# Optimization experiments

Measured on AMD Instinct MI355X. Metric: run time of the kernel, lower is better.

Reference implementation:

```python
import jax, jax.numpy as jnp
import numpy as np

N_QUBITS = 4
N_LAYERS = 2
BATCH = 1048576


def setup_inputs() -> dict:
    key = jax.random.key(0)
    k1, k2 = jax.random.split(key)
    noise = jax.random.normal(k1, (BATCH, N_QUBITS), dtype=jnp.float32)
    weights = jax.random.normal(k2, (N_LAYERS, N_QUBITS), dtype=jnp.float32)
    return {"noise": noise, "weights": weights}


def _apply_1q(state, U, wire):
    # state: (B, 2,2,2,2) complex; U: (2,2) or (B,2,2)
    s = jnp.moveaxis(state, wire + 1, -1)
    if U.ndim == 3:
        s = jnp.einsum('bij,b...j->b...i', U, s)
    else:
        s = jnp.einsum('ij,...j->...i', U, s)
    return jnp.moveaxis(s, -1, wire + 1)


def _apply_cnot(state, ctrl, tgt):
    ca, ta = ctrl + 1, tgt + 1
    s0 = jnp.take(state, 0, axis=ca)
    s1 = jnp.take(state, 1, axis=ca)
    ta_shift = ta if ta < ca else ta - 1  # target axis after removing ctrl axis
    s1 = jnp.flip(s1, axis=ta_shift)      # X on target when ctrl=1
    return jnp.stack([s0, s1], axis=ca)


def reference(noise, weights):
    B = noise.shape[0]
    # |0...0> initial state, shape (B, 2,2,2,2)
    state = jnp.zeros((B,) + (2,) * N_QUBITS, dtype=jnp.complex64)
    state = state.at[(slice(None),) + (0,) * N_QUBITS].set(1.0)

    # RX(noise[w]) on each wire (batched angles)
    for w in range(N_QUBITS):
        th = noise[:, w] * 0.5
        c, s = jnp.cos(th), jnp.sin(th)
        U = jnp.stack([jnp.stack([c + 0j, -1j * s], -1),
                       jnp.stack([-1j * s, c + 0j], -1)], -2).astype(jnp.complex64)
        state = _apply_1q(state, U, w)

    for layer in range(N_LAYERS):
        for w in range(N_QUBITS):
            state = _apply_cnot(state, w, (w + 1) % N_QUBITS)
        for w in range(N_QUBITS):
            th = weights[layer, w] * 0.5
            c, s = jnp.cos(th), jnp.sin(th)
            U = jnp.stack([jnp.stack([c, -s]), jnp.stack([s, c])]).astype(jnp.complex64)
            state = _apply_1q(state, U, w)

    probs = (state.real ** 2 + state.imag ** 2).astype(jnp.float32)
    cols = []
    for w in range(N_QUBITS):
        sum_axes = tuple(a for a in range(1, N_QUBITS + 1) if a != w + 1)
        marg = probs.sum(axis=sum_axes)  # (B, 2)
        # <Z> = p0 - p1, output = (<Z>+1)/2 = p0
        cols.append(marg[:, 0])
    return jnp.stack(cols, axis=-1)
```

## Files before the change

### kernel.cpp

```cpp
#include <hip/hip_runtime.h>
#include <math.h>


#define CNOT(cb, tb)                                                  \
    {                                                                 \
        _Pragma("unroll") for (int i = 0; i < 16; i++)                \
            if ((i & (cb)) && !(i & (tb))) {                          \
                int j = i | (tb);                                     \
                float t;                                              \
                t = re[i]; re[i] = re[j]; re[j] = t;                  \
                t = im[i]; im[i] = im[j]; im[j] = t;                  \
            }                                                         \
    }

#define RY(bit, cc, ss)                                               \
    {                                                                 \
        _Pragma("unroll") for (int i = 0; i < 16; i++)                \
            if (!(i & (bit))) {                                       \
                int j = i | (bit);                                    \
                float r0 = re[i], r1 = re[j];                         \
                float i0 = im[i], i1 = im[j];                         \
                re[i] = __builtin_fmaf((cc), r0, -((ss) * r1));       \
                re[j] = __builtin_fmaf((ss), r0, (cc) * r1);          \
                im[i] = __builtin_fmaf((cc), i0, -((ss) * i1));       \
                im[j] = __builtin_fmaf((ss), i0, (cc) * i1);          \
            }                                                         \
    }

__global__ __launch_bounds__(256) void qc_kernel(const float* __restrict__ noise,
                                                 const float* __restrict__ weights,
                                                 float* __restrict__ out, int B) {
    int b = blockIdx.x * blockDim.x + threadIdx.x;
    if (b >= B) return;

    float wc[8], wsn[8];
#pragma unroll
    for (int i = 0; i < 8; i++) {
        float th = weights[i] * 0.5f;
        __sincosf(th, &wsn[i], &wc[i]);
    }

    float4 nv = reinterpret_cast<const float4*>(noise)[b];
    float c0, s0, c1, s1, c2, s2, c3, s3;
    __sincosf(nv.x * 0.5f, &s0, &c0);
    __sincosf(nv.y * 0.5f, &s1, &c1);
    __sincosf(nv.z * 0.5f, &s2, &c2);
    __sincosf(nv.w * 0.5f, &s3, &c3);

    float m01[4], m23[4];
    m01[0] = c0 * c1; m01[1] = c0 * s1; m01[2] = s0 * c1; m01[3] = s0 * s1;
    m23[0] = c2 * c3; m23[1] = c2 * s3; m23[2] = s2 * c3; m23[3] = s2 * s3;

    float re[16], im[16];
#pragma unroll
    for (int i = 0; i < 16; i++) {
        float m = m01[i >> 2] * m23[i & 3];
        int pc = __popc(i) & 3;
        re[i] = (pc == 0) ? m : (pc == 2) ? -m : 0.0f;
        im[i] = (pc == 1) ? -m : (pc == 3) ? m : 0.0f;
    }

#pragma unroll
    for (int layer = 0; layer < 2; layer++) {
        CNOT(8, 4);
        CNOT(4, 2);
        CNOT(2, 1);
        CNOT(1, 8);
        RY(8, wc[layer * 4 + 0], wsn[layer * 4 + 0]);
        RY(4, wc[layer * 4 + 1], wsn[layer * 4 + 1]);
        RY(2, wc[layer * 4 + 2], wsn[layer * 4 + 2]);
        RY(1, wc[layer * 4 + 3], wsn[layer * 4 + 3]);
    }

    float p[16];
#pragma unroll
    for (int i = 0; i < 16; i++) p[i] = __builtin_fmaf(im[i], im[i], re[i] * re[i]);

    float g[4], h[4];
#pragma unroll
    for (int x = 0; x < 4; x++)
        g[x] = ((p[4 * x + 0] + p[4 * x + 1]) + (p[4 * x + 2] + p[4 * x + 3]));
#pragma unroll
    for (int y = 0; y < 4; y++)
        h[y] = ((p[y] + p[y + 4]) + (p[y + 8] + p[y + 12]));

    float o0 = g[0] + g[1];
    float o1 = g[0] + g[2];
    float o2 = h[0] + h[1];
    float o3 = h[0] + h[2];
    reinterpret_cast<float4*>(out)[b] = make_float4(o0, o1, o2, o3);
}

extern "C" void kernel_launch(void* const* d_in, const int* in_sizes, int n_in,
                              void* d_out, int out_size, void* d_ws, size_t ws_size,
                              hipStream_t stream) {
    const float* noise   = (const float*)d_in[0];
    const float* weights = (const float*)d_in[1];
    float* out = (float*)d_out;
    int B = in_sizes[0] / 4;

    qc_kernel<<<(B + 255) / 256, 256, 0, stream>>>(noise, weights, out, B);
}
```

Baseline: 79.88 us.

## Replace statevector simulation with closed-form expectation polynomials

Instead of simulating the 16-amplitude complex state through CNOT and RY gates, the kernel evaluates each qubit's <Z> as an analytic polynomial of the full-angle noise sines and cosines. Weight-dependent coefficients are combined into a few constants per output. This removes most per-thread arithmetic and register pressure, leaving the kernel dominated by memory traffic. The risk is correctness if the derived polynomial is wrong, and some numerical differences from reordering the arithmetic.

```diff
diff --git a/kernel.cpp b/kernel.cpp
--- a/kernel.cpp
+++ b/kernel.cpp
@@ -1,31 +1,6 @@
 #include <hip/hip_runtime.h>
 #include <math.h>
 
-
-#define CNOT(cb, tb)                                                  \
-    {                                                                 \
-        _Pragma("unroll") for (int i = 0; i < 16; i++)                \
-            if ((i & (cb)) && !(i & (tb))) {                          \
-                int j = i | (tb);                                     \
-                float t;                                              \
-                t = re[i]; re[i] = re[j]; re[j] = t;                  \
-                t = im[i]; im[i] = im[j]; im[j] = t;                  \
-            }                                                         \
-    }
-
-#define RY(bit, cc, ss)                                               \
-    {                                                                 \
-        _Pragma("unroll") for (int i = 0; i < 16; i++)                \
-            if (!(i & (bit))) {                                       \
-                int j = i | (bit);                                    \
-                float r0 = re[i], r1 = re[j];                         \
-                float i0 = im[i], i1 = im[j];                         \
-                re[i] = __builtin_fmaf((cc), r0, -((ss) * r1));       \
-                re[j] = __builtin_fmaf((ss), r0, (cc) * r1);          \
-                im[i] = __builtin_fmaf((cc), i0, -((ss) * i1));       \
-                im[j] = __builtin_fmaf((ss), i0, (cc) * i1);          \
-            }                                                         \
-    }
 
 __global__ __launch_bounds__(256) void qc_kernel(const float* __restrict__ noise,
                                                  const float* __restrict__ weights,
@@ -33,62 +8,74 @@
     int b = blockIdx.x * blockDim.x + threadIdx.x;
     if (b >= B) return;
 
-    float wc[8], wsn[8];
+    float C0[4], S0[4], C1[4], S1[4];
 #pragma unroll
-    for (int i = 0; i < 8; i++) {
-        float th = weights[i] * 0.5f;
-        __sincosf(th, &wsn[i], &wc[i]);
+    for (int v = 0; v < 4; v++) {
+        __sincosf(weights[v],     &S0[v], &C0[v]);
+        __sincosf(weights[4 + v], &S1[v], &C1[v]);
     }
 
+    float A0 = C1[0] * C0[3];
+    float K01 = A0 * C0[1] * C0[2], K02 = A0 * C0[1] * S0[2], K03 = -A0 * S0[1] * S0[2];
+    float K04 = S1[0] * C0[0] * S0[1], K05 = S1[0] * S0[0] * C0[1], K06 = -S1[0] * S0[0] * S0[1];
+
+    float K11 = C1[1] * C0[0] * C0[1], K12 = C1[1] * C0[0] * S0[1], K13 = C1[1] * S0[0] * C0[1];
+    float B1 = S1[1] * S0[2];
+    float K14 = B1 * C0[1], K15 = -B1 * S0[1];
+
+    float A2 = C1[2] * C0[0];
+    float K21 = A2 * C0[1] * C0[2], K22 = A2 * C0[1] * S0[2], K23 = -A2 * S0[1] * S0[2];
+    float K24 = -C1[2] * S0[0] * S0[1] * C0[2];
+    float B2 = S1[2] * S0[3];
+    float K25 = B2 * C0[2], K26 = -B2 * S0[2];
+
+    float A3 = C1[3] * C0[3] * C0[2];
+    float K31 = A3 * C0[0] * C0[1], K32 = A3 * C0[0] * S0[1], K33 = A3 * S0[0] * C0[1];
+    float K34 = C1[3] * C0[3] * S0[0] * S0[1] * S0[2];
+    float B3 = S1[3] * S0[3];
+    float K35 = B3 * C0[0] * C0[1], K36 = -B3 * S0[0] * S0[1];
+
     float4 nv = reinterpret_cast<const float4*>(noise)[b];
-    float c0, s0, c1, s1, c2, s2, c3, s3;
-    __sincosf(nv.x * 0.5f, &s0, &c0);
-    __sincosf(nv.y * 0.5f, &s1, &c1);
-    __sincosf(nv.z * 0.5f, &s2, &c2);
-    __sincosf(nv.w * 0.5f, &s3, &c3);
+    float z0, z1, z2, z3, y0, y1, y2, y3;
+    __sincosf(nv.x, &y0, &z0);
+    __sincosf(nv.y, &y1, &z1);
+    __sincosf(nv.z, &y2, &z2);
+    __sincosf(nv.w, &y3, &z3);
 
-    float m01[4], m23[4];
-    m01[0] = c0 * c1; m01[1] = c0 * s1; m01[2] = s0 * c1; m01[3] = s0 * s1;
-    m23[0] = c2 * c3; m23[1] = c2 * s3; m23[2] = s2 * c3; m23[3] = s2 * s3;
+    float z01 = z0 * z1, z02 = z0 * z2, z12 = z1 * z2, z13 = z1 * z3;
+    float y01 = y0 * y1, y12 = y1 * y2, y23 = y2 * y3;
+    float y02 = y0 * y2, y13 = y1 * y3, y03 = y0 * y3;
 
-    float re[16], im[16];
-#pragma unroll
-    for (int i = 0; i < 16; i++) {
-        float m = m01[i >> 2] * m23[i & 3];
-        int pc = __popc(i) & 3;
-        re[i] = (pc == 0) ? m : (pc == 2) ? -m : 0.0f;
-        im[i] = (pc == 1) ? -m : (pc == 3) ? m : 0.0f;
-    }
+    float Z0 = K01 * (z01 * z3);
+    Z0 = __builtin_fmaf(K02, y23, Z0);
+    Z0 = __builtin_fmaf(K03, z02 * y13, Z0);
+    Z0 = __builtin_fmaf(K04, y01, Z0);
+    Z0 = __builtin_fmaf(K05, y12 * z3, Z0);
+    Z0 = __builtin_fmaf(K06, z02 * z3, Z0);
 
-#pragma unroll
-    for (int layer = 0; layer < 2; layer++) {
-        CNOT(8, 4);
-        CNOT(4, 2);
-        CNOT(2, 1);
-        CNOT(1, 8);
-        RY(8, wc[layer * 4 + 0], wsn[layer * 4 + 0]);
-        RY(4, wc[layer * 4 + 1], wsn[layer * 4 + 1]);
-        RY(2, wc[layer * 4 + 2], wsn[layer * 4 + 2]);
-        RY(1, wc[layer * 4 + 3], wsn[layer * 4 + 3]);
-    }
+    float Z1 = K11 * (z02 * z3);
+    Z1 = __builtin_fmaf(K12, y12 * z3, Z1);
+    Z1 = __builtin_fmaf(K13, y01, Z1);
+    Z1 = __builtin_fmaf(K14, z0 * y12, Z1);
+    Z1 = __builtin_fmaf(K15, z2, Z1);
 
-    float p[16];
-#pragma unroll
-    for (int i = 0; i < 16; i++) p[i] = __builtin_fmaf(im[i], im[i], re[i] * re[i]);
+    float Z2 = K21 * z13;
+    Z2 = __builtin_fmaf(K22, z0 * y23, Z2);
+    Z2 = __builtin_fmaf(K23, y13 * z2, Z2);
+    Z2 = __builtin_fmaf(K24, y02 * z1, Z2);
+    Z2 = __builtin_fmaf(K25, z01 * y23, Z2);
+    Z2 = __builtin_fmaf(K26, z3, Z2);
 
-    float g[4], h[4];
-#pragma unroll
-    for (int x = 0; x < 4; x++)
-        g[x] = ((p[4 * x + 0] + p[4 * x + 1]) + (p[4 * x + 2] + p[4 * x + 3]));
-#pragma unroll
-    for (int y = 0; y < 4; y++)
-        h[y] = ((p[y] + p[y + 4]) + (p[y + 8] + p[y + 12]));
+    float Z3 = K31 * z02;
+    Z3 = __builtin_fmaf(K32, y12, Z3);
+    Z3 = __builtin_fmaf(K33, y01 * z3, Z3);
+    Z3 = __builtin_fmaf(K34, y03 * z12, Z3);
+    Z3 = __builtin_fmaf(K35, y02 * z13, Z3);
+    Z3 = __builtin_fmaf(K36, z1, Z3);
 
-    float o0 = g[0] + g[1];
-    float o1 = g[0] + g[2];
-    float o2 = h[0] + h[1];
-    float o3 = h[0] + h[2];
-    reinterpret_cast<float4*>(out)[b] = make_float4(o0, o1, o2, o3);
+    reinterpret_cast<float4*>(out)[b] =
+        make_float4(__builtin_fmaf(0.5f, Z0, 0.5f), __builtin_fmaf(0.5f, Z1, 0.5f),
+                    __builtin_fmaf(0.5f, Z2, 0.5f), __builtin_fmaf(0.5f, Z3, 0.5f));
 }
 
 extern "C" void kernel_launch(void* const* d_in, const int* in_sizes, int n_in,
```

New measurement: 70.11 us. -12.2%, faster.
